# Kernel optimization log

Measured on AMD Instinct MI355X. Metric: run time of the kernel, lower is better.

Reference implementation:

```python
import jax, jax.numpy as jnp
import numpy as np

B, N, D, H = 4, 4096, 1024, 16
DK = D // H


def setup_inputs() -> dict:
    key = jax.random.key(0)
    ks = jax.random.split(key, 11)
    s = 0.02  # small init scale for weights
    return {
        "query": jax.random.normal(ks[0], (B, N, D), jnp.float32),
        "key": jax.random.normal(ks[1], (B, N, D), jnp.float32),
        "value": jax.random.normal(ks[2], (B, N, D), jnp.float32),
        "Wq": jax.random.normal(ks[3], (D, D), jnp.float32) * s,
        "bq": jax.random.normal(ks[4], (D,), jnp.float32) * s,
        "Wk": jax.random.normal(ks[5], (D, D), jnp.float32) * s,
        "bk": jax.random.normal(ks[6], (D,), jnp.float32) * s,
        "Wv": jax.random.normal(ks[7], (D, D), jnp.float32) * s,
        "bv": jax.random.normal(ks[8], (D,), jnp.float32) * s,
        "Wo": jax.random.normal(ks[9], (D, D), jnp.float32) * s,
        "bo": jax.random.normal(ks[10], (D,), jnp.float32) * s,
    }


def reference(query, key, value, Wq, bq, Wk, bk, Wv, bv, Wo, bo):
    b, n, d = query.shape
    h, dk = H, d // H

    def proj(x, W, bias):
        # torch Linear: y = x @ W.T + b ; then split heads -> [b,h,n,dk]
        y = x @ W.T + bias
        return y.reshape(b, n, h, dk).transpose(0, 2, 1, 3)

    q = proj(query, Wq, bq)
    k = proj(key, Wk, bk)
    v = proj(value, Wv, bv)

    # linear attention (Efficient Attention, arXiv:1812.01243)
    q = jax.nn.softmax(q, axis=-1) * (1.0 / np.sqrt(dk).astype(np.float32))
    k = jax.nn.softmax(k, axis=-2)  # softmax over sequence dim
    ctx = jnp.einsum('bhnd,bhne->bhde', k, v)   # [b,h,dk,dk]
    out = jnp.einsum('bhnd,bhde->bhne', q, ctx)  # [b,h,n,dk]

    out = out.transpose(0, 2, 1, 3).reshape(b, n, d)
    return out @ Wo.T + bo
```

## Files before the change

### kernel.cpp

```cpp
#include <hip/hip_runtime.h>
#include <hip/hip_bf16.h>

#define B_ 4
#define N_ 4096
#define D_ 1024
#define H_ 16

typedef __attribute__((ext_vector_type(4))) float f32x4;
typedef __attribute__((ext_vector_type(8))) short s16x8;
typedef __attribute__((ext_vector_type(4))) unsigned int u32x4;

__device__ __forceinline__ ushort f2bf(float f) {
  union { float f; unsigned u; } v; v.f = f;
  unsigned u = v.u;
  return (ushort)((u + 0x7fffu + ((u >> 16) & 1u)) >> 16);
}

__device__ __forceinline__ void gld16(const ushort* g, ushort* lds_base) {
  __builtin_amdgcn_global_load_lds(
      (const __attribute__((address_space(1))) unsigned int*)g,
      (__attribute__((address_space(3))) unsigned int*)lds_base, 16, 0, 0);
}

__device__ __forceinline__ unsigned cvtpk(float lo, float hi) {
  unsigned r;
  asm("v_cvt_pk_bf16_f32 %0, %1, %2" : "=v"(r) : "v"(lo), "v"(hi));
  return r;
}

#define WAITVM(N) asm volatile("s_waitcnt vmcnt(" #N ")" ::: "memory")
#define LGKM0 asm volatile("s_waitcnt lgkmcnt(0)" ::: "memory")
#define SBAR __builtin_amdgcn_sched_barrier(0)
#define BARRIER __builtin_amdgcn_s_barrier()

__global__ void conv_w_kernel(const float* __restrict__ w0, const float* __restrict__ w1,
                              const float* __restrict__ w2, const float* __restrict__ w3,
                              ushort* __restrict__ dst) {
  const int z = blockIdx.z;
  const float* src = z == 0 ? w0 : z == 1 ? w1 : z == 2 ? w2 : w3;
  ushort* d = dst + (long)z * (D_ * D_);
  const long i0 = ((long)blockIdx.x * 256 + threadIdx.x) * 8;
  const long STR = (long)128 * 256 * 8;
#pragma unroll
  for (int u = 0; u < 4; ++u) {
    f32x4 a = *(const f32x4*)(src + i0 + u * STR);
    f32x4 b = *(const f32x4*)(src + i0 + u * STR + 4);
    s16x8 o;
    o[0] = (short)f2bf(a[0]); o[1] = (short)f2bf(a[1]); o[2] = (short)f2bf(a[2]); o[3] = (short)f2bf(a[3]);
    o[4] = (short)f2bf(b[0]); o[5] = (short)f2bf(b[1]); o[6] = (short)f2bf(b[2]); o[7] = (short)f2bf(b[3]);
    *(s16x8*)(d + i0 + u * STR) = o;
  }
}

template <int EPI, bool AFP32>
__global__ __launch_bounds__(512, 4) void gemm_bt_kernel(
    const void* __restrict__ Av, const ushort* __restrict__ Bm,
    void* __restrict__ Cv, const float* __restrict__ bias, float* __restrict__ kpart,
    long sA, long sB, long sC) {
  __shared__ ushort As[16384];
  __shared__ ushort Bs[16384];
  const int z = blockIdx.z;
  Bm += (long)z * sB;
  const int m0 = blockIdx.x * 128, n0 = blockIdx.y * 128;
  const int N = 1024;
  const int tid = threadIdx.x;
  const int wave = tid >> 6, lane = tid & 63;
  const int fl = lane & 15, fh = lane >> 4;
  const int wm = wave >> 1, wn = wave & 1;
  f32x4 acc[2][4] = {};

  const int rB = tid >> 2;
  const int sgB = ((tid & 3) ^ ((tid >> 3) & 3)) * 8;
  const ushort* Bp0 = Bm + (long)(n0 + rB) * 1024 + sgB;
  ushort* BsD0 = Bs + tid * 8;
  const ushort* Ab = AFP32 ? nullptr : ((const ushort*)Av + (long)z * sA);
  const ushort* Ap0 = AFP32 ? nullptr : (Ab + (long)(m0 + rB) * 1024 + sgB);
  ushort* AsD0 = As + tid * 8;
  const int ar = tid >> 2, ac = tid & 3;
  const float* apA = AFP32 ? ((const float*)Av + (long)(m0 + ar) * 1024 + ac * 8) : nullptr;
  const int awoff = ar * 32 + ((ac ^ ((tid >> 3) & 3)) * 8);
  const int fro = fl * 32 + ((fh ^ ((fl >> 1) & 3)) * 8);

  f32x4 pE0, pE1, pO0, pO1;

#define ISSUE_B(T) do { gld16(Bp0 + (T) * 32, BsD0 + (((T) & 3) << 12)); } while (0)
#define ISSUE_A16(T) do { gld16(Ap0 + (T) * 32, AsD0 + (((T) & 3) << 12)); } while (0)
#define ISSUE_AF(T, P) do { \
    P##0 = *(const f32x4*)(apA + (T) * 32); \
    P##1 = *(const f32x4*)(apA + (T) * 32 + 4); } while (0)
#define CVT_WRITE(T, P) do { \
    u32x4 _w; \
    _w[0] = cvtpk(P##0[0], P##0[1]); _w[1] = cvtpk(P##0[2], P##0[3]); \
    _w[2] = cvtpk(P##1[0], P##1[1]); _w[3] = cvtpk(P##1[2], P##1[3]); \
    *(u32x4*)(As + (((T) & 3) << 12) + awoff) = _w; } while (0)
#define MFMA_STEP(T) do { \
    const ushort* _a = As + (((T) & 3) << 12); \
    const ushort* _b = Bs + (((T) & 3) << 12); \
    s16x8 fa[2], fb[4]; \
    _Pragma("unroll") for (int i = 0; i < 2; ++i) \
      fa[i] = *(const s16x8*)(_a + (wm * 32 + i * 16) * 32 + fro); \
    _Pragma("unroll") for (int j = 0; j < 4; ++j) \
      fb[j] = *(const s16x8*)(_b + (wn * 64 + j * 16) * 32 + fro); \
    _Pragma("unroll") for (int i = 0; i < 2; ++i) \
      _Pragma("unroll") for (int j = 0; j < 4; ++j) \
        acc[i][j] = __builtin_amdgcn_mfma_f32_16x16x32_bf16(fa[i], fb[j], acc[i][j], 0, 0, 0); \
    } while (0)

  if constexpr (AFP32) {
    ISSUE_B(0); SBAR;
    ISSUE_AF(0, pE); SBAR;
    ISSUE_B(1); SBAR;
    ISSUE_AF(1, pO); SBAR;
    ISSUE_B(2); SBAR;
    CVT_WRITE(0, pE);
#pragma unroll 1
    for (int t = 0; t < 28; t += 2) {
      WAITVM(6); LGKM0; BARRIER; SBAR;
      ISSUE_AF(t + 2, pE); SBAR;
      ISSUE_B(t + 3); SBAR;
      CVT_WRITE(t + 1, pO);
      MFMA_STEP(t);
      WAITVM(6); LGKM0; BARRIER; SBAR;
      ISSUE_AF(t + 3, pO); SBAR;
      ISSUE_B(t + 4); SBAR;
      CVT_WRITE(t + 2, pE);
      MFMA_STEP(t + 1);
    }
    WAITVM(6); LGKM0; BARRIER; SBAR;
    ISSUE_AF(30, pE); SBAR;
    ISSUE_B(31); SBAR;
    CVT_WRITE(29, pO);
    MFMA_STEP(28);
    WAITVM(6); LGKM0; BARRIER; SBAR;
    ISSUE_AF(31, pO); SBAR;
    CVT_WRITE(30, pE);
    MFMA_STEP(29);
    WAITVM(5); LGKM0; BARRIER; SBAR;
    CVT_WRITE(31, pO);
    MFMA_STEP(30);
    WAITVM(2); LGKM0; BARRIER; SBAR;
    MFMA_STEP(31);
  } else {
    ISSUE_A16(0); SBAR; ISSUE_B(0); SBAR;
    ISSUE_A16(1); SBAR; ISSUE_B(1); SBAR;
    ISSUE_A16(2); SBAR; ISSUE_B(2); SBAR;
#pragma unroll 1
    for (int t = 0; t < 29; ++t) {
      WAITVM(4); BARRIER; SBAR;
      ISSUE_A16(t + 3); SBAR;
      ISSUE_B(t + 3); SBAR;
      MFMA_STEP(t);
    }
    WAITVM(4); BARRIER; SBAR; MFMA_STEP(29);
    WAITVM(2); BARRIER; SBAR; MFMA_STEP(30);
    WAITVM(0); BARRIER; SBAR; MFMA_STEP(31);
  }
#undef ISSUE_B
#undef ISSUE_A16
#undef ISSUE_AF
#undef CVT_WRITE
#undef MFMA_STEP

  if constexpr (EPI == 0) {
    ushort* C = (ushort*)Cv;
#pragma unroll
    for (int j = 0; j < 4; ++j) {
      int col = n0 + wn * 64 + j * 16 + fl;
#pragma unroll
      for (int i = 0; i < 2; ++i)
#pragma unroll
        for (int r = 0; r < 4; ++r) {
          int row = m0 + wm * 32 + i * 16 + fh * 4 + r;
          C[(long)row * N + col] = f2bf(acc[i][j][r]);
        }
    }
  } else if constexpr (EPI == 1) {
    ushort* C = (ushort*)Cv;
    float bcol[4];
#pragma unroll
    for (int j = 0; j < 4; ++j) bcol[j] = bias[n0 + wn * 64 + j * 16 + fl];
#pragma unroll
    for (int i = 0; i < 2; ++i)
#pragma unroll
      for (int r = 0; r < 4; ++r) {
        float v[4];
#pragma unroll
        for (int j = 0; j < 4; ++j) v[j] = acc[i][j][r] + bcol[j];
        float m = fmaxf(fmaxf(v[0], v[1]), fmaxf(v[2], v[3]));
#pragma unroll
        for (int o = 1; o <= 8; o <<= 1) m = fmaxf(m, __shfl_xor(m, o));
        float e[4], s = 0.f;
#pragma unroll
        for (int j = 0; j < 4; ++j) { e[j] = __expf(v[j] - m); s += e[j]; }
#pragma unroll
        for (int o = 1; o <= 8; o <<= 1) s += __shfl_xor(s, o);
        float sc = 0.125f / s;
        int row = m0 + wm * 32 + i * 16 + fh * 4 + r;
#pragma unroll
        for (int j = 0; j < 4; ++j)
          C[(long)row * N + n0 + wn * 64 + j * 16 + fl] = f2bf(e[j] * sc);
      }
  } else if constexpr (EPI == 2) {
    ushort* C = (ushort*)Cv;
    float csum[4] = {};
#pragma unroll
    for (int j = 0; j < 4; ++j) {
      int col = n0 + wn * 64 + j * 16 + fl;
#pragma unroll
      for (int i = 0; i < 2; ++i)
#pragma unroll
        for (int r = 0; r < 4; ++r) {
          int row = m0 + wm * 32 + i * 16 + fh * 4 + r;
          float e = __expf(acc[i][j][r]);
          csum[j] += e;
          C[(long)row * N + col] = f2bf(e);
        }
    }
#pragma unroll
    for (int j = 0; j < 4; ++j) {
#pragma unroll
      for (int o = 16; o <= 32; o <<= 1) csum[j] += __shfl_xor(csum[j], o);
    }
    if (fh == 0) {
      int b = m0 >> 12;
      int chunk = ((m0 & 4095) >> 7) * 4 + wm;
#pragma unroll
      for (int j = 0; j < 4; ++j)
        kpart[(long)b * 131072 + (long)chunk * 1024 + n0 + wn * 64 + j * 16 + fl] = csum[j];
    }
  } else {
    float* C = (float*)Cv + (long)z * sC;
#pragma unroll
    for (int j = 0; j < 4; ++j) {
      int col = n0 + wn * 64 + j * 16 + fl;
      float bv = bias[col];
#pragma unroll
      for (int i = 0; i < 2; ++i)
#pragma unroll
        for (int r = 0; r < 4; ++r) {
          int row = m0 + wm * 32 + i * 16 + fh * 4 + r;
          C[(long)row * N + col] = acc[i][j][r] + bv;
        }
    }
  }
}

__global__ void ksm2_kernel(const float* __restrict__ kpart, float* __restrict__ colinv) {
  int idx = blockIdx.x * 256 + threadIdx.x;
  int b = idx >> 10, d = idx & 1023;
  float s = 0.f;
  for (int c = 0; c < 128; ++c) s += kpart[(long)b * 131072 + (long)c * 1024 + d];
  colinv[idx] = 1.0f / s;
}

__global__ __launch_bounds__(256, 2) void ctx_partial_kernel(
    const ushort* __restrict__ Ksm, const ushort* __restrict__ Vp, float* __restrict__ part) {
  __shared__ ushort Ks[128 * 64];
  __shared__ ushort Vs[128 * 64];
  const int chunk = blockIdx.x;
  const int bh = blockIdx.y;
  const int b = bh >> 4, h = bh & 15;
  const int tid = threadIdx.x, wave = tid >> 6, lane = tid & 63;
  const int fl = lane & 15, fh = lane >> 4;
  f32x4 acc[4] = {};
  for (int t = 0; t < 4; ++t) {
    const long base = ((long)(b * N_ + chunk * 512 + t * 128)) * D_ + h * 64;
    __syncthreads();
#pragma unroll
    for (int i = 0; i < 4; ++i) {
      int c = i * 256 + tid;
      int r = c >> 3, k8 = (c & 7) * 8;
      ushort* lk = Ks + (long)(i * 256 + wave * 64) * 8;
      ushort* lv = Vs + (long)(i * 256 + wave * 64) * 8;
      gld16(Ksm + base + (long)r * D_ + k8, lk);
      gld16(Vp + base + (long)r * D_ + k8, lv);
    }
    __syncthreads();
#pragma unroll
    for (int s = 0; s < 4; ++s) {
      s16x8 fa;
#pragma unroll
      for (int j = 0; j < 8; ++j)
        fa[j] = (short)Ks[(s * 32 + fh * 8 + j) * 64 + wave * 16 + fl];
#pragma unroll
      for (int jt = 0; jt < 4; ++jt) {
        s16x8 fb;
#pragma unroll
        for (int j = 0; j < 8; ++j)
          fb[j] = (short)Vs[(s * 32 + fh * 8 + j) * 64 + jt * 16 + fl];
        acc[jt] = __builtin_amdgcn_mfma_f32_16x16x32_bf16(fa, fb, acc[jt], 0, 0, 0);
      }
    }
  }
  float* dst = part + ((long)chunk * 64 + bh) * 4096;
#pragma unroll
  for (int jt = 0; jt < 4; ++jt)
#pragma unroll
    for (int r = 0; r < 4; ++r)
      dst[(wave * 16 + fh * 4 + r) * 64 + jt * 16 + fl] = acc[jt][r];
}

__global__ void ctx_reduce_kernel(const float* __restrict__ part, const float* __restrict__ bv,
                                  const float* __restrict__ colinv, ushort* __restrict__ ctxb) {
  int idx = blockIdx.x * 256 + threadIdx.x;
  int e = idx & 63;
  int dk = (idx >> 6) & 63;
  int h = (idx >> 12) & 15;
  int b = idx >> 16;
  float s = 0.f;
#pragma unroll
  for (int c = 0; c < 8; ++c) s += part[(long)c * 262144 + idx];
  ctxb[idx] = f2bf(s * colinv[b * 1024 + h * 64 + dk] + bv[h * 64 + e]);
}

__global__ __launch_bounds__(256, 2) void mb_kernel(
    const ushort* __restrict__ Wob, const ushort* __restrict__ ctxb, ushort* __restrict__ Mb) {
  const int o0 = blockIdx.x * 64, h = blockIdx.y, b = blockIdx.z;
  const int tid = threadIdx.x, wave = tid >> 6, lane = tid & 63;
  const int fl = lane & 15, fh = lane >> 4;
  const ushort* ctxh = ctxb + ((long)(b * 16 + h)) * 4096;
  f32x4 acc[4] = {};
#pragma unroll
  for (int s = 0; s < 2; ++s) {
    s16x8 fa = *(const s16x8*)(Wob + (long)(o0 + wave * 16 + fl) * D_ + h * 64 + s * 32 + fh * 8);
#pragma unroll
    for (int jt = 0; jt < 4; ++jt) {
      s16x8 fb = *(const s16x8*)(ctxh + (long)(jt * 16 + fl) * 64 + s * 32 + fh * 8);
      acc[jt] = __builtin_amdgcn_mfma_f32_16x16x32_bf16(fa, fb, acc[jt], 0, 0, 0);
    }
  }
  ushort* dst = Mb + (long)b * (D_ * D_);
#pragma unroll
  for (int jt = 0; jt < 4; ++jt)
#pragma unroll
    for (int r = 0; r < 4; ++r)
      dst[(long)(o0 + wave * 16 + fh * 4 + r) * D_ + h * 64 + jt * 16 + fl] = f2bf(acc[jt][r]);
}

extern "C" void kernel_launch(void* const* d_in, const int* in_sizes, int n_in,
                              void* d_out, int out_size, void* d_ws, size_t ws_size,
                              hipStream_t stream) {
  const float* q_in = (const float*)d_in[0];
  const float* k_in = (const float*)d_in[1];
  const float* v_in = (const float*)d_in[2];
  const float* Wq = (const float*)d_in[3];
  const float* bq = (const float*)d_in[4];
  const float* Wk = (const float*)d_in[5];
  const float* Wv = (const float*)d_in[7];
  const float* bv = (const float*)d_in[8];
  const float* Wo = (const float*)d_in[9];
  const float* bo = (const float*)d_in[10];

  char* ws = (char*)d_ws;
  ushort* Wb = (ushort*)(ws + 0);
  ushort* Qp = (ushort*)(ws + 8388608);
  ushort* Kp = (ushort*)(ws + 41943040);
  ushort* Vp = (ushort*)(ws + 75497472);
  float* kpart = (float*)(ws + 109051904);
  float* colinv = (float*)(ws + 111149056);
  float* ctxpart = (float*)(ws + 111165440);
  ushort* ctxb = (ushort*)(ws + 119554048);
  ushort* Mb = (ushort*)(ws + 120078336);

  ushort* Wbq = Wb;
  ushort* Wbk = Wb + 1048576;
  ushort* Wbv = Wb + 2097152;
  ushort* Wbo = Wb + 3145728;

  conv_w_kernel<<<dim3(128, 1, 4), 256, 0, stream>>>(Wq, Wk, Wv, Wo, Wb);

  gemm_bt_kernel<1, true><<<dim3(128, 8, 1), 512, 0, stream>>>(
      q_in, Wbq, Qp, bq, nullptr, 0, 0, 0);
  gemm_bt_kernel<2, true><<<dim3(128, 8, 1), 512, 0, stream>>>(
      k_in, Wbk, Kp, nullptr, kpart, 0, 0, 0);
  gemm_bt_kernel<0, true><<<dim3(128, 8, 1), 512, 0, stream>>>(
      v_in, Wbv, Vp, nullptr, nullptr, 0, 0, 0);

  ksm2_kernel<<<16, 256, 0, stream>>>(kpart, colinv);

  ctx_partial_kernel<<<dim3(8, 64), 256, 0, stream>>>(Kp, Vp, ctxpart);
  ctx_reduce_kernel<<<1024, 256, 0, stream>>>(ctxpart, bv, colinv, ctxb);
  mb_kernel<<<dim3(16, 16, 4), 256, 0, stream>>>(Wbo, ctxb, Mb);

  gemm_bt_kernel<3, false><<<dim3(32, 8, 4), 512, 0, stream>>>(
      Qp, Mb, (float*)d_out, bo, nullptr,
      (long)4096 * 1024, (long)1024 * 1024, (long)4096 * 1024);
}
```

Baseline: 302.6 us.

## Enlarge GEMM block tile to 256x256 with triple-buffered fp32 A prefetch

Grows the bf16 MFMA GEMM block tile from 128x128 to 256x256, so each wave now computes a 128x64 sub-tile. This halves how often A and B tiles are reloaded from global memory, and each loaded B fragment is reused across eight A fragments. The fp32 A input is prefetched three stages ahead in a register ring and the MFMA section is wrapped in s_setprio. The k-softmax partial sums and workspace offsets are resized to match. In exchange it doubles LDS to 128KB per block and grows the accumulator count. That allows only one block per CU, leaves only 256 blocks in the projection grids, and risks register spills.

```diff
diff --git a/kernel.cpp b/kernel.cpp
--- a/kernel.cpp
+++ b/kernel.cpp
@@ -53,111 +53,124 @@
 }
 
 template <int EPI, bool AFP32>
-__global__ __launch_bounds__(512, 4) void gemm_bt_kernel(
+__global__ __launch_bounds__(512, 2) void gemm_bt_kernel(
     const void* __restrict__ Av, const ushort* __restrict__ Bm,
     void* __restrict__ Cv, const float* __restrict__ bias, float* __restrict__ kpart,
     long sA, long sB, long sC) {
-  __shared__ ushort As[16384];
-  __shared__ ushort Bs[16384];
+  __shared__ ushort As[32768];
+  __shared__ ushort Bs[32768];
   const int z = blockIdx.z;
   Bm += (long)z * sB;
-  const int m0 = blockIdx.x * 128, n0 = blockIdx.y * 128;
+  const int m0 = blockIdx.x * 256, n0 = blockIdx.y * 256;
   const int N = 1024;
   const int tid = threadIdx.x;
-  const int wave = tid >> 6, lane = tid & 63;
+  const int lane = tid & 63;
+  const int wave = tid >> 6;
   const int fl = lane & 15, fh = lane >> 4;
-  const int wm = wave >> 1, wn = wave & 1;
-  f32x4 acc[2][4] = {};
-
-  const int rB = tid >> 2;
-  const int sgB = ((tid & 3) ^ ((tid >> 3) & 3)) * 8;
-  const ushort* Bp0 = Bm + (long)(n0 + rB) * 1024 + sgB;
-  ushort* BsD0 = Bs + tid * 8;
+  const int wm = wave >> 2, wn = wave & 3;
+  f32x4 acc[8][4] = {};
+
+  const int fro = (fh ^ ((fl >> 1) & 3)) * 8;
+  const int rmb = (wm * 128 + fl) * 32;
+  const int rnb = (wn * 64 + fl) * 32;
+
+  const int brow = tid >> 2;
+  const int bslot = ((tid & 3) ^ ((brow >> 1) & 3)) * 8;
+  const ushort* Bsrc0 = Bm + (long)(n0 + brow) * 1024 + bslot;
+  const ushort* Bsrc1 = Bm + (long)(n0 + brow + 128) * 1024 + bslot;
+
   const ushort* Ab = AFP32 ? nullptr : ((const ushort*)Av + (long)z * sA);
-  const ushort* Ap0 = AFP32 ? nullptr : (Ab + (long)(m0 + rB) * 1024 + sgB);
-  ushort* AsD0 = As + tid * 8;
-  const int ar = tid >> 2, ac = tid & 3;
-  const float* apA = AFP32 ? ((const float*)Av + (long)(m0 + ar) * 1024 + ac * 8) : nullptr;
-  const int awoff = ar * 32 + ((ac ^ ((tid >> 3) & 3)) * 8);
-  const int fro = fl * 32 + ((fh ^ ((fl >> 1) & 3)) * 8);
-
-  f32x4 pE0, pE1, pO0, pO1;
-
-#define ISSUE_B(T) do { gld16(Bp0 + (T) * 32, BsD0 + (((T) & 3) << 12)); } while (0)
-#define ISSUE_A16(T) do { gld16(Ap0 + (T) * 32, AsD0 + (((T) & 3) << 12)); } while (0)
-#define ISSUE_AF(T, P) do { \
-    P##0 = *(const f32x4*)(apA + (T) * 32); \
-    P##1 = *(const f32x4*)(apA + (T) * 32 + 4); } while (0)
-#define CVT_WRITE(T, P) do { \
-    u32x4 _w; \
-    _w[0] = cvtpk(P##0[0], P##0[1]); _w[1] = cvtpk(P##0[2], P##0[3]); \
-    _w[2] = cvtpk(P##1[0], P##1[1]); _w[3] = cvtpk(P##1[2], P##1[3]); \
-    *(u32x4*)(As + (((T) & 3) << 12) + awoff) = _w; } while (0)
+  const ushort* Asrc0 = AFP32 ? nullptr : (Ab + (long)(m0 + brow) * 1024 + bslot);
+  const ushort* Asrc1 = AFP32 ? nullptr : (Ab + (long)(m0 + brow + 128) * 1024 + bslot);
+
+  const int ar = tid >> 1, ch = tid & 1;
+  const float* apA = AFP32 ? ((const float*)Av + (long)(m0 + ar) * 1024 + ch * 16) : nullptr;
+  const int aw0 = ar * 32 + (((ch * 2) ^ ((ar >> 1) & 3)) * 8);
+  const int aw1 = ar * 32 + (((ch * 2 + 1) ^ ((ar >> 1) & 3)) * 8);
+
+  f32x4 q0_0, q0_1, q0_2, q0_3;
+  f32x4 q1_0, q1_1, q1_2, q1_3;
+  f32x4 q2_0, q2_1, q2_2, q2_3;
+
+#define ISSUE_B(T) do { \
+    gld16(Bsrc0 + (T) * 32, Bs + (((T) & 3) << 13) + tid * 8); \
+    gld16(Bsrc1 + (T) * 32, Bs + (((T) & 3) << 13) + tid * 8 + 4096); } while (0)
+#define ISSUE_A16(T) do { \
+    gld16(Asrc0 + (T) * 32, As + (((T) & 3) << 13) + tid * 8); \
+    gld16(Asrc1 + (T) * 32, As + (((T) & 3) << 13) + tid * 8 + 4096); } while (0)
+#define ISSUE_P(T, S) do { \
+    S##_0 = *(const f32x4*)(apA + (T) * 32); \
+    S##_1 = *(const f32x4*)(apA + (T) * 32 + 4); \
+    S##_2 = *(const f32x4*)(apA + (T) * 32 + 8); \
+    S##_3 = *(const f32x4*)(apA + (T) * 32 + 12); } while (0)
+#define CVT_WRITE(T, S) do { \
+    u32x4 _w0, _w1; \
+    _w0[0] = cvtpk(S##_0[0], S##_0[1]); _w0[1] = cvtpk(S##_0[2], S##_0[3]); \
+    _w0[2] = cvtpk(S##_1[0], S##_1[1]); _w0[3] = cvtpk(S##_1[2], S##_1[3]); \
+    _w1[0] = cvtpk(S##_2[0], S##_2[1]); _w1[1] = cvtpk(S##_2[2], S##_2[3]); \
+    _w1[2] = cvtpk(S##_3[0], S##_3[1]); _w1[3] = cvtpk(S##_3[2], S##_3[3]); \
+    *(u32x4*)(As + (((T) & 3) << 13) + aw0) = _w0; \
+    *(u32x4*)(As + (((T) & 3) << 13) + aw1) = _w1; } while (0)
 #define MFMA_STEP(T) do { \
-    const ushort* _a = As + (((T) & 3) << 12); \
-    const ushort* _b = Bs + (((T) & 3) << 12); \
-    s16x8 fa[2], fb[4]; \
-    _Pragma("unroll") for (int i = 0; i < 2; ++i) \
-      fa[i] = *(const s16x8*)(_a + (wm * 32 + i * 16) * 32 + fro); \
+    const ushort* _a = As + (((T) & 3) << 13); \
+    const ushort* _b = Bs + (((T) & 3) << 13); \
+    s16x8 fb[4]; \
     _Pragma("unroll") for (int j = 0; j < 4; ++j) \
-      fb[j] = *(const s16x8*)(_b + (wn * 64 + j * 16) * 32 + fro); \
-    _Pragma("unroll") for (int i = 0; i < 2; ++i) \
+      fb[j] = *(const s16x8*)(_b + rnb + j * 512 + fro); \
+    __builtin_amdgcn_s_setprio(1); \
+    _Pragma("unroll") for (int i = 0; i < 8; ++i) { \
+      s16x8 fa = *(const s16x8*)(_a + rmb + i * 512 + fro); \
       _Pragma("unroll") for (int j = 0; j < 4; ++j) \
-        acc[i][j] = __builtin_amdgcn_mfma_f32_16x16x32_bf16(fa[i], fb[j], acc[i][j], 0, 0, 0); \
-    } while (0)
+        acc[i][j] = __builtin_amdgcn_mfma_f32_16x16x32_bf16(fa, fb[j], acc[i][j], 0, 0, 0); \
+    } \
+    __builtin_amdgcn_s_setprio(0); } while (0)
 
   if constexpr (AFP32) {
-    ISSUE_B(0); SBAR;
-    ISSUE_AF(0, pE); SBAR;
-    ISSUE_B(1); SBAR;
-    ISSUE_AF(1, pO); SBAR;
-    ISSUE_B(2); SBAR;
-    CVT_WRITE(0, pE);
+    ISSUE_B(0); ISSUE_P(0, q0);
+    ISSUE_B(1); ISSUE_P(1, q1);
+    ISSUE_B(2); ISSUE_P(2, q2);
+    CVT_WRITE(0, q0);
+#define STEP_F(T, SW, SR) do { \
+    WAITVM(16); LGKM0; BARRIER; SBAR; \
+    ISSUE_B((T) + 3); ISSUE_P((T) + 3, SW); SBAR; \
+    MFMA_STEP(T); \
+    CVT_WRITE((T) + 1, SR); } while (0)
 #pragma unroll 1
-    for (int t = 0; t < 28; t += 2) {
-      WAITVM(6); LGKM0; BARRIER; SBAR;
-      ISSUE_AF(t + 2, pE); SBAR;
-      ISSUE_B(t + 3); SBAR;
-      CVT_WRITE(t + 1, pO);
-      MFMA_STEP(t);
-      WAITVM(6); LGKM0; BARRIER; SBAR;
-      ISSUE_AF(t + 3, pO); SBAR;
-      ISSUE_B(t + 4); SBAR;
-      CVT_WRITE(t + 2, pE);
-      MFMA_STEP(t + 1);
-    }
-    WAITVM(6); LGKM0; BARRIER; SBAR;
-    ISSUE_AF(30, pE); SBAR;
-    ISSUE_B(31); SBAR;
-    CVT_WRITE(29, pO);
-    MFMA_STEP(28);
-    WAITVM(6); LGKM0; BARRIER; SBAR;
-    ISSUE_AF(31, pO); SBAR;
-    CVT_WRITE(30, pE);
-    MFMA_STEP(29);
-    WAITVM(5); LGKM0; BARRIER; SBAR;
-    CVT_WRITE(31, pO);
-    MFMA_STEP(30);
-    WAITVM(2); LGKM0; BARRIER; SBAR;
+    for (int t = 0; t < 27; t += 3) {
+      STEP_F(t, q0, q1);
+      STEP_F(t + 1, q1, q2);
+      STEP_F(t + 2, q2, q0);
+    }
+    WAITVM(16); LGKM0; BARRIER; SBAR;
+    ISSUE_B(30); ISSUE_P(30, q0); SBAR;
+    MFMA_STEP(27); CVT_WRITE(28, q1);
+    WAITVM(16); LGKM0; BARRIER; SBAR;
+    ISSUE_B(31); ISSUE_P(31, q1); SBAR;
+    MFMA_STEP(28); CVT_WRITE(29, q2);
+    WAITVM(16); LGKM0; BARRIER; SBAR;
+    MFMA_STEP(29); CVT_WRITE(30, q0);
+    WAITVM(10); LGKM0; BARRIER; SBAR;
+    MFMA_STEP(30); CVT_WRITE(31, q1);
+    WAITVM(0); LGKM0; BARRIER; SBAR;
     MFMA_STEP(31);
+#undef STEP_F
   } else {
-    ISSUE_A16(0); SBAR; ISSUE_B(0); SBAR;
-    ISSUE_A16(1); SBAR; ISSUE_B(1); SBAR;
-    ISSUE_A16(2); SBAR; ISSUE_B(2); SBAR;
+    ISSUE_A16(0); ISSUE_B(0);
+    ISSUE_A16(1); ISSUE_B(1);
+    ISSUE_A16(2); ISSUE_B(2);
 #pragma unroll 1
     for (int t = 0; t < 29; ++t) {
-      WAITVM(4); BARRIER; SBAR;
-      ISSUE_A16(t + 3); SBAR;
-      ISSUE_B(t + 3); SBAR;
+      WAITVM(8); LGKM0; BARRIER; SBAR;
+      ISSUE_A16(t + 3); ISSUE_B(t + 3); SBAR;
       MFMA_STEP(t);
     }
-    WAITVM(4); BARRIER; SBAR; MFMA_STEP(29);
-    WAITVM(2); BARRIER; SBAR; MFMA_STEP(30);
-    WAITVM(0); BARRIER; SBAR; MFMA_STEP(31);
+    WAITVM(8); LGKM0; BARRIER; SBAR; MFMA_STEP(29);
+    WAITVM(4); LGKM0; BARRIER; SBAR; MFMA_STEP(30);
+    WAITVM(0); LGKM0; BARRIER; SBAR; MFMA_STEP(31);
   }
 #undef ISSUE_B
 #undef ISSUE_A16
-#undef ISSUE_AF
+#undef ISSUE_P
 #undef CVT_WRITE
 #undef MFMA_STEP
 
@@ -167,10 +180,10 @@
     for (int j = 0; j < 4; ++j) {
       int col = n0 + wn * 64 + j * 16 + fl;
 #pragma unroll
-      for (int i = 0; i < 2; ++i)
+      for (int i = 0; i < 8; ++i)
 #pragma unroll
         for (int r = 0; r < 4; ++r) {
-          int row = m0 + wm * 32 + i * 16 + fh * 4 + r;
+          int row = m0 + wm * 128 + i * 16 + fh * 4 + r;
           C[(long)row * N + col] = f2bf(acc[i][j][r]);
         }
     }
@@ -180,7 +193,7 @@
 #pragma unroll
     for (int j = 0; j < 4; ++j) bcol[j] = bias[n0 + wn * 64 + j * 16 + fl];
 #pragma unroll
-    for (int i = 0; i < 2; ++i)
+    for (int i = 0; i < 8; ++i)
 #pragma unroll
       for (int r = 0; r < 4; ++r) {
         float v[4];
@@ -195,7 +208,7 @@
 #pragma unroll
         for (int o = 1; o <= 8; o <<= 1) s += __shfl_xor(s, o);
         float sc = 0.125f / s;
-        int row = m0 + wm * 32 + i * 16 + fh * 4 + r;
+        int row = m0 + wm * 128 + i * 16 + fh * 4 + r;
 #pragma unroll
         for (int j = 0; j < 4; ++j)
           C[(long)row * N + n0 + wn * 64 + j * 16 + fl] = f2bf(e[j] * sc);
@@ -207,10 +220,10 @@
     for (int j = 0; j < 4; ++j) {
       int col = n0 + wn * 64 + j * 16 + fl;
 #pragma unroll
-      for (int i = 0; i < 2; ++i)
+      for (int i = 0; i < 8; ++i)
 #pragma unroll
         for (int r = 0; r < 4; ++r) {
-          int row = m0 + wm * 32 + i * 16 + fh * 4 + r;
+          int row = m0 + wm * 128 + i * 16 + fh * 4 + r;
           float e = __expf(acc[i][j][r]);
           csum[j] += e;
           C[(long)row * N + col] = f2bf(e);
@@ -223,10 +236,10 @@
     }
     if (fh == 0) {
       int b = m0 >> 12;
-      int chunk = ((m0 & 4095) >> 7) * 4 + wm;
+      int chunk = ((m0 & 4095) >> 7) + wm;
 #pragma unroll
       for (int j = 0; j < 4; ++j)
-        kpart[(long)b * 131072 + (long)chunk * 1024 + n0 + wn * 64 + j * 16 + fl] = csum[j];
+        kpart[(long)b * 32768 + (long)chunk * 1024 + n0 + wn * 64 + j * 16 + fl] = csum[j];
     }
   } else {
     float* C = (float*)Cv + (long)z * sC;
@@ -235,10 +248,10 @@
       int col = n0 + wn * 64 + j * 16 + fl;
       float bv = bias[col];
 #pragma unroll
-      for (int i = 0; i < 2; ++i)
+      for (int i = 0; i < 8; ++i)
 #pragma unroll
         for (int r = 0; r < 4; ++r) {
-          int row = m0 + wm * 32 + i * 16 + fh * 4 + r;
+          int row = m0 + wm * 128 + i * 16 + fh * 4 + r;
           C[(long)row * N + col] = acc[i][j][r] + bv;
         }
     }
@@ -249,7 +262,7 @@
   int idx = blockIdx.x * 256 + threadIdx.x;
   int b = idx >> 10, d = idx & 1023;
   float s = 0.f;
-  for (int c = 0; c < 128; ++c) s += kpart[(long)b * 131072 + (long)c * 1024 + d];
+  for (int c = 0; c < 32; ++c) s += kpart[(long)b * 32768 + (long)c * 1024 + d];
   colinv[idx] = 1.0f / s;
 }
 
@@ -357,10 +370,10 @@
   ushort* Kp = (ushort*)(ws + 41943040);
   ushort* Vp = (ushort*)(ws + 75497472);
   float* kpart = (float*)(ws + 109051904);
-  float* colinv = (float*)(ws + 111149056);
-  float* ctxpart = (float*)(ws + 111165440);
-  ushort* ctxb = (ushort*)(ws + 119554048);
-  ushort* Mb = (ushort*)(ws + 120078336);
+  float* colinv = (float*)(ws + 109576192);
+  float* ctxpart = (float*)(ws + 109592576);
+  ushort* ctxb = (ushort*)(ws + 117981184);
+  ushort* Mb = (ushort*)(ws + 118505472);
 
   ushort* Wbq = Wb;
   ushort* Wbk = Wb + 1048576;
@@ -369,11 +382,11 @@
 
   conv_w_kernel<<<dim3(128, 1, 4), 256, 0, stream>>>(Wq, Wk, Wv, Wo, Wb);
 
-  gemm_bt_kernel<1, true><<<dim3(128, 8, 1), 512, 0, stream>>>(
+  gemm_bt_kernel<1, true><<<dim3(64, 4, 1), 512, 0, stream>>>(
       q_in, Wbq, Qp, bq, nullptr, 0, 0, 0);
-  gemm_bt_kernel<2, true><<<dim3(128, 8, 1), 512, 0, stream>>>(
+  gemm_bt_kernel<2, true><<<dim3(64, 4, 1), 512, 0, stream>>>(
       k_in, Wbk, Kp, nullptr, kpart, 0, 0, 0);
-  gemm_bt_kernel<0, true><<<dim3(128, 8, 1), 512, 0, stream>>>(
+  gemm_bt_kernel<0, true><<<dim3(64, 4, 1), 512, 0, stream>>>(
       v_in, Wbv, Vp, nullptr, nullptr, 0, 0, 0);
 
   ksm2_kernel<<<16, 256, 0, stream>>>(kpart, colinv);
@@ -382,7 +395,7 @@
   ctx_reduce_kernel<<<1024, 256, 0, stream>>>(ctxpart, bv, colinv, ctxb);
   mb_kernel<<<dim3(16, 16, 4), 256, 0, stream>>>(Wbo, ctxb, Mb);
 
-  gemm_bt_kernel<3, false><<<dim3(32, 8, 4), 512, 0, stream>>>(
+  gemm_bt_kernel<3, false><<<dim3(16, 4, 4), 512, 0, stream>>>(
       Qp, Mb, (float*)d_out, bo, nullptr,
       (long)4096 * 1024, (long)1024 * 1024, (long)4096 * 1024);
 }
```

Result: slower. 317.9 us (+5.1%).
